# Optimization experiments

Measured on AMD Instinct MI355X. Metric: run time of the kernel, lower is better.

Reference implementation:

```python
import jax, jax.numpy as jnp
import numpy as np

T, N, E = 8, 5000, 160000
IN_DIM, HID, H = 64, 128, 8
D = HID // H  # head dim = 16
NC = 2
EPS = 1e-5


def layer_norm(x, g, b):
    mu = jnp.mean(x, axis=-1, keepdims=True)
    var = jnp.mean((x - mu) ** 2, axis=-1, keepdims=True)
    return (x - mu) / jnp.sqrt(var + EPS) * g + b


def setup_inputs() -> dict:
    key = jax.random.key(0)
    ks = jax.random.split(key, 24)
    p = {}
    p["x"] = jax.random.normal(ks[0], (T, N, IN_DIM), dtype=jnp.float32)
    p["edge_index"] = jax.random.randint(ks[1], (T, 2, E), 0, N, dtype=jnp.int32)
    p["noise"] = jax.random.normal(ks[2], (N, HID), dtype=jnp.float32)
    def w(k, shape, fan_in):
        return jax.random.normal(k, shape, dtype=jnp.float32) * (1.0 / np.sqrt(fan_in))
    p["W_proj"] = w(ks[3], (IN_DIM, HID), IN_DIM)
    p["b_proj"] = jnp.zeros((HID,), jnp.float32)
    p["W_gat"] = w(ks[4], (HID, HID), HID)
    p["a_src"] = w(ks[5], (H, D), D)
    p["a_dst"] = w(ks[6], (H, D), D)
    p["b_gat"] = jnp.zeros((HID,), jnp.float32)
    p["g1"] = jnp.ones((HID,), jnp.float32)
    p["be1"] = jnp.zeros((HID,), jnp.float32)
    p["W_qkv"] = w(ks[7], (3 * HID, HID), HID)
    p["b_qkv"] = jnp.zeros((3 * HID,), jnp.float32)
    p["W_o"] = w(ks[8], (HID, HID), HID)
    p["b_o"] = jnp.zeros((HID,), jnp.float32)
    p["g2"] = jnp.ones((HID,), jnp.float32)
    p["be2"] = jnp.zeros((HID,), jnp.float32)
    p["Wc1"] = w(ks[9], (HID, HID), HID)
    p["bc1"] = jnp.zeros((HID,), jnp.float32)
    p["gc"] = jnp.ones((HID,), jnp.float32)
    p["bec"] = jnp.zeros((HID,), jnp.float32)
    p["Wc2"] = w(ks[10], (HID, NC), HID)
    p["bc2"] = jnp.array([0.0, 0.1], jnp.float32)
    return p


def reference(x, edge_index, noise, W_proj, b_proj, W_gat, a_src, a_dst, b_gat,
              g1, be1, W_qkv, b_qkv, W_o, b_o, g2, be2,
              Wc1, bc1, gc, bec, Wc2, bc2):
    # per-timestep projection + ReLU: [T, N, HID]
    h = jax.nn.relu(x @ W_proj + b_proj)

    loop = jnp.arange(N, dtype=edge_index.dtype)

    def gat(h_t, ei):  # h_t: [N, HID], ei: [2, E]
        src = jnp.concatenate([ei[0], loop])  # add self loops
        dst = jnp.concatenate([ei[1], loop])
        xh = (h_t @ W_gat).reshape(N, H, D)          # [N, H, D]
        a_s = jnp.sum(xh * a_src, axis=-1)           # [N, H]
        a_d = jnp.sum(xh * a_dst, axis=-1)           # [N, H]
        e = jax.nn.leaky_relu(a_s[src] + a_d[dst], 0.2)  # [E', H]
        m = jax.ops.segment_max(e, dst, num_segments=N)
        ex = jnp.exp(e - m[dst])
        s = jax.ops.segment_sum(ex, dst, num_segments=N)
        alpha = ex / (s[dst] + 1e-16)                # segment softmax per dst/head
        out = jax.ops.segment_sum(xh[src] * alpha[..., None], dst, num_segments=N)
        return out.reshape(N, HID) + b_gat

    feats = jax.vmap(gat)(h, edge_index)             # [T, N, HID]
    nf = jnp.transpose(feats, (1, 0, 2))             # [N, T, HID] (node = batch)

    nrm = layer_norm(nf, g1, be1)
    qkv = nrm @ W_qkv.T + b_qkv                      # [N, T, 3*HID]
    q, k, v = jnp.split(qkv, 3, axis=-1)
    def heads(t):
        return t.reshape(N, T, H, D).transpose(0, 2, 1, 3)  # [N, H, T, D]
    q, k, v = heads(q), heads(k), heads(v)
    scores = jnp.einsum('nhqd,nhkd->nhqk', q, k) / jnp.sqrt(jnp.float32(D))
    attn = jax.nn.softmax(scores, axis=-1)
    ta = jnp.einsum('nhqk,nhkd->nhqd', attn, v)
    ta = ta.transpose(0, 2, 1, 3).reshape(N, T, HID) @ W_o.T + b_o

    fused = layer_norm(nf + ta, g2, be2)
    emb = fused[:, -1, :]                            # [N, HID]

    node_ids = jnp.arange(N, dtype=jnp.float32) / N
    div = jnp.sin(node_ids * 6.28) * 0.1             # [N]
    emb = emb + div[:, None] + noise * 0.05          # eval noise scale

    h1 = emb @ Wc1 + bc1
    h1 = jax.nn.gelu(layer_norm(h1, gc, bec), approximate=False)
    logits = h1 @ Wc2 + bc2                          # [N, 2]
    sinu = jnp.sin(jnp.arange(N, dtype=jnp.float32) * 0.5) * 0.2
    logits = logits.at[:, 1].add(sinu)
    return emb, logits
```

## Files before the change

kernel.cpp:

```cpp
#include <hip/hip_runtime.h>
#include <math.h>

#define T 8
#define N 5000
#define E 160000
#define EN (E + N)
#define IN_DIM 64
#define HID 128
#define H 8
#define D 16
#define NC 2
#define MT 32
#define NB 4
#define NRR 8
#define NCHK 32
#define RSZ ((N + NRR - 1) / NRR)
#define CSZ ((EN + NCHK - 1) / NCHK)

__device__ __forceinline__ float leaky(float e) { return (e >= 0.0f) ? e : 0.2f * e; }

__global__ __launch_bounds__(256) void k_pg(const float* __restrict__ x,
                                            const float* __restrict__ Wp,
                                            const float* __restrict__ bp,
                                            const float* __restrict__ Wg,
                                            const float* __restrict__ asrc,
                                            const float* __restrict__ adst,
                                            float* __restrict__ xh,
                                            float* __restrict__ a_s,
                                            float* __restrict__ a_d,
                                            int* __restrict__ cursor) {
    __shared__ float xt[MT][IN_DIM];
    __shared__ float ht[MT][HID + 1];
    int row0 = blockIdx.x * MT;
    int tid = threadIdx.x;

    {
        int gi = blockIdx.x * 256 + tid;
        if (gi < T * N) cursor[gi] = 0;
    }

    for (int idx = tid; idx < MT * IN_DIM; idx += 256) {
        int r = idx >> 6, k = idx & 63;
        xt[r][k] = x[(size_t)(row0 + r) * IN_DIM + k];
    }
    __syncthreads();

    int cg = tid & 31;
    int rg = tid >> 5;
    int c0 = cg * 4, r0 = rg * 4;

    {
        float4 b4 = *(const float4*)(bp + c0);
        float a00=b4.x,a01=b4.y,a02=b4.z,a03=b4.w;
        float a10=b4.x,a11=b4.y,a12=b4.z,a13=b4.w;
        float a20=b4.x,a21=b4.y,a22=b4.z,a23=b4.w;
        float a30=b4.x,a31=b4.y,a32=b4.z,a33=b4.w;
        for (int k = 0; k < IN_DIM; ++k) {
            float4 w = *(const float4*)(Wp + (size_t)k * HID + c0);
            float x0 = xt[r0 + 0][k], x1 = xt[r0 + 1][k];
            float x2 = xt[r0 + 2][k], x3 = xt[r0 + 3][k];
            a00 += x0*w.x; a01 += x0*w.y; a02 += x0*w.z; a03 += x0*w.w;
            a10 += x1*w.x; a11 += x1*w.y; a12 += x1*w.z; a13 += x1*w.w;
            a20 += x2*w.x; a21 += x2*w.y; a22 += x2*w.z; a23 += x2*w.w;
            a30 += x3*w.x; a31 += x3*w.y; a32 += x3*w.z; a33 += x3*w.w;
        }
        ht[r0+0][c0+0]=fmaxf(a00,0.f); ht[r0+0][c0+1]=fmaxf(a01,0.f);
        ht[r0+0][c0+2]=fmaxf(a02,0.f); ht[r0+0][c0+3]=fmaxf(a03,0.f);
        ht[r0+1][c0+0]=fmaxf(a10,0.f); ht[r0+1][c0+1]=fmaxf(a11,0.f);
        ht[r0+1][c0+2]=fmaxf(a12,0.f); ht[r0+1][c0+3]=fmaxf(a13,0.f);
        ht[r0+2][c0+0]=fmaxf(a20,0.f); ht[r0+2][c0+1]=fmaxf(a21,0.f);
        ht[r0+2][c0+2]=fmaxf(a22,0.f); ht[r0+2][c0+3]=fmaxf(a23,0.f);
        ht[r0+3][c0+0]=fmaxf(a30,0.f); ht[r0+3][c0+1]=fmaxf(a31,0.f);
        ht[r0+3][c0+2]=fmaxf(a32,0.f); ht[r0+3][c0+3]=fmaxf(a33,0.f);
    }
    __syncthreads();

    float a00=0,a01=0,a02=0,a03=0, a10=0,a11=0,a12=0,a13=0;
    float a20=0,a21=0,a22=0,a23=0, a30=0,a31=0,a32=0,a33=0;
    for (int k = 0; k < HID; ++k) {
        float4 w = *(const float4*)(Wg + (size_t)k * HID + c0);
        float h0 = ht[r0 + 0][k], h1 = ht[r0 + 1][k];
        float h2 = ht[r0 + 2][k], h3 = ht[r0 + 3][k];
        a00 += h0*w.x; a01 += h0*w.y; a02 += h0*w.z; a03 += h0*w.w;
        a10 += h1*w.x; a11 += h1*w.y; a12 += h1*w.z; a13 += h1*w.w;
        a20 += h2*w.x; a21 += h2*w.y; a22 += h2*w.z; a23 += h2*w.w;
        a30 += h3*w.x; a31 += h3*w.y; a32 += h3*w.z; a33 += h3*w.w;
    }
    {
        float4 v;
        v.x=a00; v.y=a01; v.z=a02; v.w=a03;
        *(float4*)(xh + (size_t)(row0 + r0 + 0) * HID + c0) = v;
        v.x=a10; v.y=a11; v.z=a12; v.w=a13;
        *(float4*)(xh + (size_t)(row0 + r0 + 1) * HID + c0) = v;
        v.x=a20; v.y=a21; v.z=a22; v.w=a23;
        *(float4*)(xh + (size_t)(row0 + r0 + 2) * HID + c0) = v;
        v.x=a30; v.y=a31; v.z=a32; v.w=a33;
        *(float4*)(xh + (size_t)(row0 + r0 + 3) * HID + c0) = v;
    }
    __syncthreads();
    ht[r0+0][c0+0]=a00; ht[r0+0][c0+1]=a01; ht[r0+0][c0+2]=a02; ht[r0+0][c0+3]=a03;
    ht[r0+1][c0+0]=a10; ht[r0+1][c0+1]=a11; ht[r0+1][c0+2]=a12; ht[r0+1][c0+3]=a13;
    ht[r0+2][c0+0]=a20; ht[r0+2][c0+1]=a21; ht[r0+2][c0+2]=a22; ht[r0+2][c0+3]=a23;
    ht[r0+3][c0+0]=a30; ht[r0+3][c0+1]=a31; ht[r0+3][c0+2]=a32; ht[r0+3][c0+3]=a33;
    __syncthreads();

    {
        int r = tid >> 3, hh = tid & 7;
        float s1 = 0.0f, s2 = 0.0f;
        #pragma unroll
        for (int d = 0; d < D; ++d) {
            float v = ht[r][hh * D + d];
            s1 += v * asrc[hh * D + d];
            s2 += v * adst[hh * D + d];
        }
        a_s[(size_t)(row0 + r) * H + hh] = s1;
        a_d[(size_t)(row0 + r) * H + hh] = s2;
    }
}

__global__ void k_tr(const float* __restrict__ W_qkv, const float* __restrict__ W_o,
                     float* __restrict__ WTq, float* __restrict__ WoT) {
    int idx = blockIdx.x * 256 + threadIdx.x;
    if (idx < 384 * 128) {
        int j = idx >> 7, c = idx & 127;
        WTq[c * 384 + j] = W_qkv[idx];
    } else if (idx < 384 * 128 + 128 * 128) {
        int r = idx - 384 * 128;
        int j = r >> 7, k = r & 127;
        WoT[k * 128 + j] = W_o[r];
    }
}

__global__ __launch_bounds__(256) void k_hist(const int* __restrict__ ei,
                                              int* __restrict__ cursor) {
    __shared__ int hist[N];
    int t = blockIdx.x >> 3;
    int chunk = blockIdx.x & 7;
    int tid = threadIdx.x;

    for (int i = tid; i < N; i += 256) hist[i] = 0;
    __syncthreads();

    const int CS = (EN + 7) / 8;
    int i0 = chunk * CS;
    int i1 = (i0 + CS < EN) ? i0 + CS : EN;
    const int* drow = ei + (size_t)(2 * t + 1) * E;
    for (int i = i0 + tid; i < i1; i += 256) {
        int d = (i < E) ? drow[i] : (i - E);
        atomicAdd(&hist[d], 1);
    }
    __syncthreads();

    int* cur = cursor + t * N;
    for (int i = tid; i < N; i += 256) {
        int c = hist[i];
        if (c) atomicAdd(&cur[i], c);
    }
}

__global__ void k_scan(int* __restrict__ cursor, int* __restrict__ offs) {
    __shared__ int part[256];
    int t = blockIdx.x;
    int tid = threadIdx.x;
    const int CH = 20;
    int begin = tid * CH;
    int sum = 0;
    for (int k = 0; k < CH; ++k) {
        int i = begin + k;
        if (i < N) sum += cursor[t * N + i];
    }
    part[tid] = sum;
    __syncthreads();
    if (tid == 0) {
        int run = 0;
        for (int i = 0; i < 256; ++i) { int v = part[i]; part[i] = run; run += v; }
        offs[t * (N + 1) + N] = run;
    }
    __syncthreads();
    int run = part[tid];
    for (int k = 0; k < CH; ++k) {
        int i = begin + k;
        if (i < N) {
            int cnt = cursor[t * N + i];
            offs[t * (N + 1) + i] = run;
            cursor[t * N + i] = run;
            run += cnt;
        }
    }
}

__global__ __launch_bounds__(256) void k_scatter(const int* __restrict__ ei,
                                                 int* __restrict__ cursor,
                                                 int* __restrict__ csr_src) {
    int idx = blockIdx.x;
    int g = idx & 63;
    int c = idx >> 6;
    int t = g >> 3;
    int r = g & 7;
    int lo = r * RSZ;
    int hi = (lo + RSZ < N) ? lo + RSZ : N;
    int i0 = c * CSZ;
    int i1 = (i0 + CSZ < EN) ? i0 + CSZ : EN;

    const int* srow = ei + (size_t)(2 * t) * E;
    const int* drow = srow + E;
    int* cur = cursor + t * N;
    int* csb = csr_src + (size_t)t * EN;

    for (int i = i0 + threadIdx.x; i < i1; i += 256) {
        int s, d;
        if (i < E) { d = drow[i]; s = srow[i]; }
        else       { s = d = i - E; }
        if (d >= lo && d < hi) {
            int pos = atomicAdd(&cur[d], 1);
            csb[pos] = s;
        }
    }
}

__global__ __launch_bounds__(128) void k_aggc(
        const int* __restrict__ offs, const int* __restrict__ csr_src,
        const float* __restrict__ a_s, const float* __restrict__ a_d,
        const float* __restrict__ xh, const float* __restrict__ b_gat,
        const float* __restrict__ g1, const float* __restrict__ be1,
        float* __restrict__ nrm, float* __restrict__ xlast_g) {
    int b = blockIdx.x;
    int t = b & 7;
    int dst = b >> 3;
    int tid = threadIdx.x;

    int o0 = offs[t * (N + 1) + dst];
    int o1 = offs[t * (N + 1) + dst + 1];
    int deg = o1 - o0;
    const int* esrc = csr_src + (size_t)t * EN + o0;
    const float* as_b = a_s + (size_t)t * N * H;
    const float* ad_b = a_d + (size_t)t * N * H;
    const float* xh_b = xh + (size_t)t * N * HID;

    __shared__ float lal[16][H];
    __shared__ int   lsrc[16];
    __shared__ float ws_s[2][H];
    __shared__ float pacc[2][HID];
    __shared__ float red[128];

    int eh_e = tid >> 3, eh_h = tid & 7;
    int el = tid >> 5, cg = tid & 31;
    int hg = cg >> 2;
    float adh_e = ad_b[dst * H + eh_h];

    float4 acc = {0.0f, 0.0f, 0.0f, 0.0f};
    float wpart = 0.0f;

    int ntile = (deg + 15) >> 4;
    for (int tt = 0; tt < ntile; ++tt) {
        int ej = (tt << 4) + eh_e;
        float w = 0.0f;
        int src = 0;
        if (ej < deg) {
            src = esrc[ej];
            w = expf(leaky(as_b[src * H + eh_h] + adh_e));
        }
        if (eh_h == 0) lsrc[eh_e] = src;
        lal[eh_e][eh_h] = w;
        wpart += w;
        __syncthreads();
        #pragma unroll
        for (int jj = 0; jj < 4; ++jj) {
            int j = (jj << 2) + el;
            int s = lsrc[j];
            float l = lal[j][hg];
            float4 v = *(const float4*)(xh_b + (size_t)s * HID + (cg << 2));
            acc.x += l * v.x; acc.y += l * v.y;
            acc.z += l * v.z; acc.w += l * v.w;
        }
        __syncthreads();
    }

    {
        float w = wpart;
        w += __shfl_xor(w, 8);
        w += __shfl_xor(w, 16);
        w += __shfl_xor(w, 32);
        if ((tid & 63) < 8) ws_s[tid >> 6][eh_h] = w;
    }
    acc.x += __shfl_xor(acc.x, 32);
    acc.y += __shfl_xor(acc.y, 32);
    acc.z += __shfl_xor(acc.z, 32);
    acc.w += __shfl_xor(acc.w, 32);
    if (!(tid & 32)) *(float4*)&pacc[tid >> 6][(tid & 31) << 2] = acc;
    __syncthreads();

    int hh = tid >> 4;
    float wsum = ws_s[0][hh] + ws_s[1][hh];
    float val = (pacc[0][tid] + pacc[1][tid]) / (wsum + 1e-16f);

    float v = val + b_gat[tid];
    red[tid] = v;
    __syncthreads();
    if (tid < 64) {
        float s = red[tid] + red[tid + 64];
        #pragma unroll
        for (int m = 1; m < 64; m <<= 1) s += __shfl_xor(s, m);
        if (tid == 0) red[0] = s;
    }
    __syncthreads();
    float mu = red[0] * (1.0f / HID);
    __syncthreads();
    float dv = v - mu;
    red[tid] = dv * dv;
    __syncthreads();
    if (tid < 64) {
        float s = red[tid] + red[tid + 64];
        #pragma unroll
        for (int m = 1; m < 64; m <<= 1) s += __shfl_xor(s, m);
        if (tid == 0) red[0] = s;
    }
    __syncthreads();
    float rstd = rsqrtf(red[0] * (1.0f / HID) + 1e-5f);

    nrm[(size_t)(dst * T + t) * HID + tid] = dv * rstd * g1[tid] + be1[tid];
    if (t == T - 1) xlast_g[(size_t)dst * HID + tid] = v;
}

__global__ __launch_bounds__(256) void k_fuse(
        const float* __restrict__ nrm,
        const float* __restrict__ WTq,
        const float* __restrict__ b_qkv,
        const float* __restrict__ xlast_g,
        const float* __restrict__ WoT,
        const float* __restrict__ b_o,
        const float* __restrict__ g2, const float* __restrict__ be2,
        const float* __restrict__ noise, float* __restrict__ out) {
    __shared__ float at[NB * T][HID];
    __shared__ float ql[NB][HID];
    __shared__ float ws[8][384];
    float* ta_s = &at[0][0];

    int n0 = blockIdx.x * NB;
    int tid = threadIdx.x;
    int cg = tid & 31, rg = tid >> 5;
    int c0 = cg * 4, r0 = rg * 4;
    int u = rg >> 1;

    {
        const float* srcp = nrm + (size_t)n0 * T * HID;
        for (int idx = tid; idx < NB * T * 32; idx += 256) {
            int r = idx >> 5, c4 = (idx & 31) << 2;
            *(float4*)&at[r][c4] = *(const float4*)(srcp + (size_t)r * HID + c4);
        }
    }

    float ka[4][4], va[4][4], qa[4];
    {
        float4 bk = *(const float4*)(b_qkv + 128 + c0);
        float4 bv = *(const float4*)(b_qkv + 256 + c0);
        #pragma unroll
        for (int i = 0; i < 4; ++i) {
            ka[i][0] = bk.x; ka[i][1] = bk.y; ka[i][2] = bk.z; ka[i][3] = bk.w;
            va[i][0] = bv.x; va[i][1] = bv.y; va[i][2] = bv.z; va[i][3] = bv.w;
        }
        if (rg < 4) {
            float4 bq = *(const float4*)(b_qkv + c0);
            qa[0] = bq.x; qa[1] = bq.y; qa[2] = bq.z; qa[3] = bq.w;
        } else {
            qa[0] = qa[1] = qa[2] = qa[3] = 0.0f;
        }
    }

    int f1 = 256 + tid, f2 = 512 + tid;
    int sr0 = tid / 96,  sc0 = (tid - sr0 * 96) << 2;
    int sr1 = f1 / 96,   sc1 = (f1 - sr1 * 96) << 2;
    int sr2 = f2 / 96,   sc2 = (f2 - sr2 * 96) << 2;
    const float* wp0 = WTq + (size_t)sr0 * 384 + sc0;
    const float* wp1 = WTq + (size_t)sr1 * 384 + sc1;
    const float* wp2 = WTq + (size_t)sr2 * 384 + sc2;
    float4 wr0 = *(const float4*)wp0;
    float4 wr1 = *(const float4*)wp1;
    float4 wr2 = *(const float4*)wp2;
    __syncthreads();

    const float* atq = at[(rg & 3) * T + (T - 1)];

    for (int kc = 0; kc < 16; ++kc) {
        if (kc) __syncthreads();
        *(float4*)&ws[sr0][sc0] = wr0;
        *(float4*)&ws[sr1][sc1] = wr1;
        *(float4*)&ws[sr2][sc2] = wr2;
        if (kc < 15) {
            int off = (kc + 1) * 8 * 384;
            wr0 = *(const float4*)(wp0 + off);
            wr1 = *(const float4*)(wp1 + off);
            wr2 = *(const float4*)(wp2 + off);
        }
        __syncthreads();

        #pragma unroll
        for (int kk = 0; kk < 8; kk += 4) {
            int k = kc * 8 + kk;
            float4 e0 = *(const float4*)&at[r0 + 0][k];
            float4 e1 = *(const float4*)&at[r0 + 1][k];
            float4 e2 = *(const float4*)&at[r0 + 2][k];
            float4 e3 = *(const float4*)&at[r0 + 3][k];
            float e0a[4] = {e0.x, e0.y, e0.z, e0.w};
            float e1a[4] = {e1.x, e1.y, e1.z, e1.w};
            float e2a[4] = {e2.x, e2.y, e2.z, e2.w};
            float e3a[4] = {e3.x, e3.y, e3.z, e3.w};
            float eqa[4] = {0.f, 0.f, 0.f, 0.f};
            if (rg < 4) {
                float4 eq = *(const float4*)&atq[k];
                eqa[0] = eq.x; eqa[1] = eq.y; eqa[2] = eq.z; eqa[3] = eq.w;
            }
            #pragma unroll
            for (int j = 0; j < 4; ++j) {
                float4 wk = *(const float4*)&ws[kk + j][128 + c0];
                float4 wv = *(const float4*)&ws[kk + j][256 + c0];
                float x0 = e0a[j], x1 = e1a[j], x2 = e2a[j], x3 = e3a[j];
                ka[0][0] += x0*wk.x; ka[0][1] += x0*wk.y; ka[0][2] += x0*wk.z; ka[0][3] += x0*wk.w;
                ka[1][0] += x1*wk.x; ka[1][1] += x1*wk.y; ka[1][2] += x1*wk.z; ka[1][3] += x1*wk.w;
                ka[2][0] += x2*wk.x; ka[2][1] += x2*wk.y; ka[2][2] += x2*wk.z; ka[2][3] += x2*wk.w;
                ka[3][0] += x3*wk.x; ka[3][1] += x3*wk.y; ka[3][2] += x3*wk.z; ka[3][3] += x3*wk.w;
                va[0][0] += x0*wv.x; va[0][1] += x0*wv.y; va[0][2] += x0*wv.z; va[0][3] += x0*wv.w;
                va[1][0] += x1*wv.x; va[1][1] += x1*wv.y; va[1][2] += x1*wv.z; va[1][3] += x1*wv.w;
                va[2][0] += x2*wv.x; va[2][1] += x2*wv.y; va[2][2] += x2*wv.z; va[2][3] += x2*wv.w;
                va[3][0] += x3*wv.x; va[3][1] += x3*wv.y; va[3][2] += x3*wv.z; va[3][3] += x3*wv.w;
                if (rg < 4) {
                    float4 wq = *(const float4*)&ws[kk + j][c0];
                    float xq = eqa[j];
                    qa[0] += xq*wq.x; qa[1] += xq*wq.y; qa[2] += xq*wq.z; qa[3] += xq*wq.w;
                }
            }
        }
    }
    __syncthreads();

    if (rg < 4) {
        float4 q4; q4.x = qa[0]; q4.y = qa[1]; q4.z = qa[2]; q4.w = qa[3];
        *(float4*)&ql[rg][c0] = q4;
    }
    __syncthreads();

    float p0, p1, p2, p3;
    {
        float4 q4 = *(const float4*)&ql[u][c0];
        float ps[4];
        #pragma unroll
        for (int i = 0; i < 4; ++i) {
            float s = q4.x * ka[i][0] + q4.y * ka[i][1]
                    + q4.z * ka[i][2] + q4.w * ka[i][3];
            s += __shfl_xor(s, 1);
            s += __shfl_xor(s, 2);
            ps[i] = s * 0.25f;
        }
        float mx = fmaxf(fmaxf(ps[0], ps[1]), fmaxf(ps[2], ps[3]));
        mx = fmaxf(mx, __shfl_xor(mx, 32));
        float e0 = expf(ps[0] - mx), e1 = expf(ps[1] - mx);
        float e2 = expf(ps[2] - mx), e3 = expf(ps[3] - mx);
        float ssum = e0 + e1 + e2 + e3;
        ssum += __shfl_xor(ssum, 32);
        float inv = 1.0f / ssum;
        p0 = (e0 * va[0][0] + e1 * va[1][0] + e2 * va[2][0] + e3 * va[3][0]) * inv;
        p1 = (e0 * va[0][1] + e1 * va[1][1] + e2 * va[2][1] + e3 * va[3][1]) * inv;
        p2 = (e0 * va[0][2] + e1 * va[1][2] + e2 * va[2][2] + e3 * va[3][2]) * inv;
        p3 = (e0 * va[0][3] + e1 * va[1][3] + e2 * va[2][3] + e3 * va[3][3]) * inv;
        p0 += __shfl_xor(p0, 32);
        p1 += __shfl_xor(p1, 32);
        p2 += __shfl_xor(p2, 32);
        p3 += __shfl_xor(p3, 32);
    }
    if (!(tid & 32)) {
        float4 t4; t4.x = p0; t4.y = p1; t4.z = p2; t4.w = p3;
        *(float4*)&ta_s[u * 128 + c0] = t4;
    }
    __syncthreads();

    {
        int uu = tid >> 6, c = tid & 63;
        int n = n0 + uu;
        float o0 = b_o[c], o1 = b_o[c + 64];
        const float* tar = ta_s + uu * 128;
        #pragma unroll 8
        for (int k = 0; k < HID; k += 4) {
            float t0 = tar[k], t1 = tar[k+1], t2 = tar[k+2], t3 = tar[k+3];
            o0 += t0 * WoT[(size_t)(k+0)*128 + c]  + t1 * WoT[(size_t)(k+1)*128 + c]
                + t2 * WoT[(size_t)(k+2)*128 + c]  + t3 * WoT[(size_t)(k+3)*128 + c];
            o1 += t0 * WoT[(size_t)(k+0)*128 + c+64] + t1 * WoT[(size_t)(k+1)*128 + c+64]
                + t2 * WoT[(size_t)(k+2)*128 + c+64] + t3 * WoT[(size_t)(k+3)*128 + c+64];
        }
        float xa = xlast_g[(size_t)n * HID + c];
        float xb = xlast_g[(size_t)n * HID + c + 64];
        float x2a = xa + o0, x2b = xb + o1;
        float s = x2a + x2b, qs = x2a * x2a + x2b * x2b;
        #pragma unroll
        for (int m = 1; m < 64; m <<= 1) {
            s  += __shfl_xor(s, m);
            qs += __shfl_xor(qs, m);
        }
        float mu = s * (1.0f / HID);
        float var = qs * (1.0f / HID) - mu * mu;
        float rstd = rsqrtf(var + 1e-5f);
        float dv = sinf(((float)n / (float)N) * 6.28f) * 0.1f;
        out[(size_t)n * HID + c] =
            (x2a - mu) * rstd * g2[c] + be2[c] + dv
            + noise[(size_t)n * HID + c] * 0.05f;
        out[(size_t)n * HID + c + 64] =
            (x2b - mu) * rstd * g2[c + 64] + be2[c + 64] + dv
            + noise[(size_t)n * HID + c + 64] * 0.05f;
    }
}

__global__ __launch_bounds__(256) void k_cls(const float* __restrict__ emb,
                                             const float* __restrict__ Wc1,
                                             const float* __restrict__ bc1,
                                             const float* __restrict__ gc,
                                             const float* __restrict__ bec,
                                             const float* __restrict__ Wc2,
                                             const float* __restrict__ bc2,
                                             float* __restrict__ out) {
    __shared__ float et[MT][HID];
    __shared__ float h1t[MT][HID + 1];
    int row0 = blockIdx.x * MT;
    int tid = threadIdx.x;

    for (int idx = tid; idx < MT * HID; idx += 256) {
        int r = idx >> 7, c = idx & 127;
        int row = row0 + r;
        et[r][c] = (row < N) ? emb[(size_t)row * HID + c] : 0.0f;
    }
    __syncthreads();

    {
        int cg = tid & 31, rg = tid >> 5;
        int c0 = cg * 4, r0 = rg * 4;
        float4 b4 = *(const float4*)(bc1 + c0);
        float a00=b4.x,a01=b4.y,a02=b4.z,a03=b4.w;
        float a10=b4.x,a11=b4.y,a12=b4.z,a13=b4.w;
        float a20=b4.x,a21=b4.y,a22=b4.z,a23=b4.w;
        float a30=b4.x,a31=b4.y,a32=b4.z,a33=b4.w;
        for (int k = 0; k < HID; ++k) {
            float4 w = *(const float4*)(Wc1 + (size_t)k * HID + c0);
            float e0 = et[r0 + 0][k], e1 = et[r0 + 1][k];
            float e2 = et[r0 + 2][k], e3 = et[r0 + 3][k];
            a00 += e0*w.x; a01 += e0*w.y; a02 += e0*w.z; a03 += e0*w.w;
            a10 += e1*w.x; a11 += e1*w.y; a12 += e1*w.z; a13 += e1*w.w;
            a20 += e2*w.x; a21 += e2*w.y; a22 += e2*w.z; a23 += e2*w.w;
            a30 += e3*w.x; a31 += e3*w.y; a32 += e3*w.z; a33 += e3*w.w;
        }
        h1t[r0+0][c0+0]=a00; h1t[r0+0][c0+1]=a01; h1t[r0+0][c0+2]=a02; h1t[r0+0][c0+3]=a03;
        h1t[r0+1][c0+0]=a10; h1t[r0+1][c0+1]=a11; h1t[r0+1][c0+2]=a12; h1t[r0+1][c0+3]=a13;
        h1t[r0+2][c0+0]=a20; h1t[r0+2][c0+1]=a21; h1t[r0+2][c0+2]=a22; h1t[r0+2][c0+3]=a23;
        h1t[r0+3][c0+0]=a30; h1t[r0+3][c0+1]=a31; h1t[r0+3][c0+2]=a32; h1t[r0+3][c0+3]=a33;
    }
    __syncthreads();

    {
        int r = tid >> 3, l = tid & 7;
        float p = 0.0f;
        #pragma unroll
        for (int k = 0; k < 16; ++k) p += h1t[r][l + 8 * k];
        #pragma unroll
        for (int m = 1; m < 8; m <<= 1) p += __shfl_xor(p, m);
        float mu = p * (1.0f / HID);
        float v = 0.0f;
        #pragma unroll
        for (int k = 0; k < 16; ++k) { float d = h1t[r][l + 8 * k] - mu; v += d * d; }
        #pragma unroll
        for (int m = 1; m < 8; m <<= 1) v += __shfl_xor(v, m);
        float rstd = rsqrtf(v * (1.0f / HID) + 1e-5f);
        #pragma unroll
        for (int k = 0; k < 16; ++k) {
            int c = l + 8 * k;
            float lnv = (h1t[r][c] - mu) * rstd * gc[c] + bec[c];
            h1t[r][c] = 0.5f * lnv * (1.0f + erff(lnv * 0.70710678118f));
        }
    }
    __syncthreads();

    if (tid < MT * NC) {
        int r = tid >> 1, j = tid & 1;
        int row = row0 + r;
        if (row < N) {
            float acc = bc2[j];
            #pragma unroll 8
            for (int c = 0; c < HID; ++c) acc += h1t[r][c] * Wc2[c * NC + j];
            if (j == 1) acc += sinf((float)row * 0.5f) * 0.2f;
            out[(size_t)N * HID + (size_t)row * NC + j] = acc;
        }
    }
}

extern "C" void kernel_launch(void* const* d_in, const int* in_sizes, int n_in,
                              void* d_out, int out_size, void* d_ws, size_t ws_size,
                              hipStream_t stream) {
    const float* x      = (const float*)d_in[0];
    const int*   ei     = (const int*)d_in[1];
    const float* noise  = (const float*)d_in[2];
    const float* W_proj = (const float*)d_in[3];
    const float* b_proj = (const float*)d_in[4];
    const float* W_gat  = (const float*)d_in[5];
    const float* a_src  = (const float*)d_in[6];
    const float* a_dst  = (const float*)d_in[7];
    const float* b_gat  = (const float*)d_in[8];
    const float* g1     = (const float*)d_in[9];
    const float* be1    = (const float*)d_in[10];
    const float* W_qkv  = (const float*)d_in[11];
    const float* b_qkv  = (const float*)d_in[12];
    const float* W_o    = (const float*)d_in[13];
    const float* b_o    = (const float*)d_in[14];
    const float* g2     = (const float*)d_in[15];
    const float* be2    = (const float*)d_in[16];
    const float* Wc1    = (const float*)d_in[17];
    const float* bc1    = (const float*)d_in[18];
    const float* gc     = (const float*)d_in[19];
    const float* bec    = (const float*)d_in[20];
    const float* Wc2    = (const float*)d_in[21];
    const float* bc2    = (const float*)d_in[22];
    float* out = (float*)d_out;

    float* xh     = (float*)d_ws;
    float* nrm    = xh + 5120000;
    float* a_s    = nrm + 5120000;
    float* a_d    = a_s + 320000;
    int*   offs    = (int*)(a_d + 320000);
    int*   cursor  = offs + 40008;
    int*   csr_src = cursor + 40000;
    float* WTq    = (float*)(csr_src + 1320000);
    float* WoT    = WTq + 49152;
    float* xlastg = WoT + 16384;

    k_tr<<<(384 * 128 + 128 * 128 + 255) / 256, 256, 0, stream>>>(W_qkv, W_o, WTq, WoT);

    k_pg<<<T * N / MT, 256, 0, stream>>>(x, W_proj, b_proj, W_gat, a_src, a_dst,
                                         xh, a_s, a_d, cursor);

    k_hist<<<T * 8, 256, 0, stream>>>(ei, cursor);
    k_scan<<<T, 256, 0, stream>>>(cursor, offs);
    k_scatter<<<64 * NCHK, 256, 0, stream>>>(ei, cursor, csr_src);

    k_aggc<<<T * N, 128, 0, stream>>>(offs, csr_src, a_s, a_d, xh,
                                      b_gat, g1, be1, nrm, xlastg);

    k_fuse<<<N / NB, 256, 0, stream>>>(nrm, WTq, b_qkv, xlastg, WoT, b_o,
                                       g2, be2, noise, out);

    k_cls<<<(N + MT - 1) / MT, 256, 0, stream>>>(out, Wc1, bc1, gc, bec, Wc2, bc2, out);
}
```

Before: 372.9 us.

## Process eight nodes per block in fused attention with one warp per node

The fused temporal-attention kernel now handles 8 nodes per block, with each 32-lane warp owning one node and all T timesteps. Each thread keeps K/V accumulators for all 8 timesteps plus Q for the last one, so the q staging buffer, its extra syncs and the cross-half-wave shuffles go away. The output projection and layernorm now use float4 loads and stores, one warp per node. The register-prefetched weight staging is dropped in favour of direct loads followed by a sync, which may expose global latency and raise register pressure (about 68 accumulators per thread). It also halves the grid size.

```diff
diff --git a/kernel.cpp b/kernel.cpp
--- a/kernel.cpp
+++ b/kernel.cpp
@@ -11,7 +11,7 @@
 #define D 16
 #define NC 2
 #define MT 32
-#define NB 4
+#define NB 8
 #define NRR 8
 #define NCHK 32
 #define RSZ ((N + NRR - 1) / NRR)
@@ -332,15 +332,14 @@
         const float* __restrict__ g2, const float* __restrict__ be2,
         const float* __restrict__ noise, float* __restrict__ out) {
     __shared__ float at[NB * T][HID];
-    __shared__ float ql[NB][HID];
     __shared__ float ws[8][384];
     float* ta_s = &at[0][0];
 
     int n0 = blockIdx.x * NB;
     int tid = threadIdx.x;
     int cg = tid & 31, rg = tid >> 5;
-    int c0 = cg * 4, r0 = rg * 4;
-    int u = rg >> 1;
+    int c0 = cg * 4;
+    int r0 = rg * T;
 
     {
         const float* srcp = nrm + (size_t)n0 * T * HID;
@@ -350,161 +349,115 @@
         }
     }
 
-    float ka[4][4], va[4][4], qa[4];
+    float ka[T][4], va[T][4], qa[4];
     {
         float4 bk = *(const float4*)(b_qkv + 128 + c0);
         float4 bv = *(const float4*)(b_qkv + 256 + c0);
-        #pragma unroll
-        for (int i = 0; i < 4; ++i) {
+        float4 bq = *(const float4*)(b_qkv + c0);
+        #pragma unroll
+        for (int i = 0; i < T; ++i) {
             ka[i][0] = bk.x; ka[i][1] = bk.y; ka[i][2] = bk.z; ka[i][3] = bk.w;
             va[i][0] = bv.x; va[i][1] = bv.y; va[i][2] = bv.z; va[i][3] = bv.w;
         }
-        if (rg < 4) {
-            float4 bq = *(const float4*)(b_qkv + c0);
-            qa[0] = bq.x; qa[1] = bq.y; qa[2] = bq.z; qa[3] = bq.w;
-        } else {
-            qa[0] = qa[1] = qa[2] = qa[3] = 0.0f;
-        }
-    }
-
-    int f1 = 256 + tid, f2 = 512 + tid;
-    int sr0 = tid / 96,  sc0 = (tid - sr0 * 96) << 2;
-    int sr1 = f1 / 96,   sc1 = (f1 - sr1 * 96) << 2;
-    int sr2 = f2 / 96,   sc2 = (f2 - sr2 * 96) << 2;
-    const float* wp0 = WTq + (size_t)sr0 * 384 + sc0;
-    const float* wp1 = WTq + (size_t)sr1 * 384 + sc1;
-    const float* wp2 = WTq + (size_t)sr2 * 384 + sc2;
-    float4 wr0 = *(const float4*)wp0;
-    float4 wr1 = *(const float4*)wp1;
-    float4 wr2 = *(const float4*)wp2;
-    __syncthreads();
-
-    const float* atq = at[(rg & 3) * T + (T - 1)];
+        qa[0] = bq.x; qa[1] = bq.y; qa[2] = bq.z; qa[3] = bq.w;
+    }
 
     for (int kc = 0; kc < 16; ++kc) {
-        if (kc) __syncthreads();
-        *(float4*)&ws[sr0][sc0] = wr0;
-        *(float4*)&ws[sr1][sc1] = wr1;
-        *(float4*)&ws[sr2][sc2] = wr2;
-        if (kc < 15) {
-            int off = (kc + 1) * 8 * 384;
-            wr0 = *(const float4*)(wp0 + off);
-            wr1 = *(const float4*)(wp1 + off);
-            wr2 = *(const float4*)(wp2 + off);
+        #pragma unroll
+        for (int j = 0; j < 3; ++j) {
+            int f = j * 256 + tid;
+            int row = f / 96;
+            int cc = (f - row * 96) << 2;
+            *(float4*)&ws[row][cc] =
+                *(const float4*)(WTq + (size_t)(kc * 8 + row) * 384 + cc);
         }
         __syncthreads();
 
         #pragma unroll
-        for (int kk = 0; kk < 8; kk += 4) {
-            int k = kc * 8 + kk;
-            float4 e0 = *(const float4*)&at[r0 + 0][k];
-            float4 e1 = *(const float4*)&at[r0 + 1][k];
-            float4 e2 = *(const float4*)&at[r0 + 2][k];
-            float4 e3 = *(const float4*)&at[r0 + 3][k];
-            float e0a[4] = {e0.x, e0.y, e0.z, e0.w};
-            float e1a[4] = {e1.x, e1.y, e1.z, e1.w};
-            float e2a[4] = {e2.x, e2.y, e2.z, e2.w};
-            float e3a[4] = {e3.x, e3.y, e3.z, e3.w};
-            float eqa[4] = {0.f, 0.f, 0.f, 0.f};
-            if (rg < 4) {
-                float4 eq = *(const float4*)&atq[k];
-                eqa[0] = eq.x; eqa[1] = eq.y; eqa[2] = eq.z; eqa[3] = eq.w;
-            }
+        for (int kk = 0; kk < 8; ++kk) {
+            float4 wk = *(const float4*)&ws[kk][128 + c0];
+            float4 wv = *(const float4*)&ws[kk][256 + c0];
+            float4 wq = *(const float4*)&ws[kk][c0];
+            const float* atc = &at[r0][0] + kc * 8 + kk;
             #pragma unroll
-            for (int j = 0; j < 4; ++j) {
-                float4 wk = *(const float4*)&ws[kk + j][128 + c0];
-                float4 wv = *(const float4*)&ws[kk + j][256 + c0];
-                float x0 = e0a[j], x1 = e1a[j], x2 = e2a[j], x3 = e3a[j];
-                ka[0][0] += x0*wk.x; ka[0][1] += x0*wk.y; ka[0][2] += x0*wk.z; ka[0][3] += x0*wk.w;
-                ka[1][0] += x1*wk.x; ka[1][1] += x1*wk.y; ka[1][2] += x1*wk.z; ka[1][3] += x1*wk.w;
-                ka[2][0] += x2*wk.x; ka[2][1] += x2*wk.y; ka[2][2] += x2*wk.z; ka[2][3] += x2*wk.w;
-                ka[3][0] += x3*wk.x; ka[3][1] += x3*wk.y; ka[3][2] += x3*wk.z; ka[3][3] += x3*wk.w;
-                va[0][0] += x0*wv.x; va[0][1] += x0*wv.y; va[0][2] += x0*wv.z; va[0][3] += x0*wv.w;
-                va[1][0] += x1*wv.x; va[1][1] += x1*wv.y; va[1][2] += x1*wv.z; va[1][3] += x1*wv.w;
-                va[2][0] += x2*wv.x; va[2][1] += x2*wv.y; va[2][2] += x2*wv.z; va[2][3] += x2*wv.w;
-                va[3][0] += x3*wv.x; va[3][1] += x3*wv.y; va[3][2] += x3*wv.z; va[3][3] += x3*wv.w;
-                if (rg < 4) {
-                    float4 wq = *(const float4*)&ws[kk + j][c0];
-                    float xq = eqa[j];
-                    qa[0] += xq*wq.x; qa[1] += xq*wq.y; qa[2] += xq*wq.z; qa[3] += xq*wq.w;
+            for (int i = 0; i < T; ++i) {
+                float x = atc[i * HID];
+                ka[i][0] += x*wk.x; ka[i][1] += x*wk.y;
+                ka[i][2] += x*wk.z; ka[i][3] += x*wk.w;
+                va[i][0] += x*wv.x; va[i][1] += x*wv.y;
+                va[i][2] += x*wv.z; va[i][3] += x*wv.w;
+                if (i == T - 1) {
+                    qa[0] += x*wq.x; qa[1] += x*wq.y;
+                    qa[2] += x*wq.z; qa[3] += x*wq.w;
                 }
             }
         }
-    }
-    __syncthreads();
-
-    if (rg < 4) {
-        float4 q4; q4.x = qa[0]; q4.y = qa[1]; q4.z = qa[2]; q4.w = qa[3];
-        *(float4*)&ql[rg][c0] = q4;
-    }
-    __syncthreads();
-
-    float p0, p1, p2, p3;
-    {
-        float4 q4 = *(const float4*)&ql[u][c0];
-        float ps[4];
-        #pragma unroll
-        for (int i = 0; i < 4; ++i) {
-            float s = q4.x * ka[i][0] + q4.y * ka[i][1]
-                    + q4.z * ka[i][2] + q4.w * ka[i][3];
+        __syncthreads();
+    }
+
+    {
+        float ps[T];
+        #pragma unroll
+        for (int t = 0; t < T; ++t) {
+            float s = qa[0]*ka[t][0] + qa[1]*ka[t][1]
+                    + qa[2]*ka[t][2] + qa[3]*ka[t][3];
             s += __shfl_xor(s, 1);
             s += __shfl_xor(s, 2);
-            ps[i] = s * 0.25f;
-        }
-        float mx = fmaxf(fmaxf(ps[0], ps[1]), fmaxf(ps[2], ps[3]));
-        mx = fmaxf(mx, __shfl_xor(mx, 32));
-        float e0 = expf(ps[0] - mx), e1 = expf(ps[1] - mx);
-        float e2 = expf(ps[2] - mx), e3 = expf(ps[3] - mx);
-        float ssum = e0 + e1 + e2 + e3;
-        ssum += __shfl_xor(ssum, 32);
+            ps[t] = s * 0.25f;
+        }
+        float mx = ps[0];
+        #pragma unroll
+        for (int t = 1; t < T; ++t) mx = fmaxf(mx, ps[t]);
+        float ssum = 0.0f;
+        float ex[T];
+        #pragma unroll
+        for (int t = 0; t < T; ++t) { ex[t] = expf(ps[t] - mx); ssum += ex[t]; }
         float inv = 1.0f / ssum;
-        p0 = (e0 * va[0][0] + e1 * va[1][0] + e2 * va[2][0] + e3 * va[3][0]) * inv;
-        p1 = (e0 * va[0][1] + e1 * va[1][1] + e2 * va[2][1] + e3 * va[3][1]) * inv;
-        p2 = (e0 * va[0][2] + e1 * va[1][2] + e2 * va[2][2] + e3 * va[3][2]) * inv;
-        p3 = (e0 * va[0][3] + e1 * va[1][3] + e2 * va[2][3] + e3 * va[3][3]) * inv;
-        p0 += __shfl_xor(p0, 32);
-        p1 += __shfl_xor(p1, 32);
-        p2 += __shfl_xor(p2, 32);
-        p3 += __shfl_xor(p3, 32);
-    }
-    if (!(tid & 32)) {
-        float4 t4; t4.x = p0; t4.y = p1; t4.z = p2; t4.w = p3;
-        *(float4*)&ta_s[u * 128 + c0] = t4;
-    }
-    __syncthreads();
-
-    {
-        int uu = tid >> 6, c = tid & 63;
-        int n = n0 + uu;
-        float o0 = b_o[c], o1 = b_o[c + 64];
-        const float* tar = ta_s + uu * 128;
-        #pragma unroll 8
-        for (int k = 0; k < HID; k += 4) {
-            float t0 = tar[k], t1 = tar[k+1], t2 = tar[k+2], t3 = tar[k+3];
-            o0 += t0 * WoT[(size_t)(k+0)*128 + c]  + t1 * WoT[(size_t)(k+1)*128 + c]
-                + t2 * WoT[(size_t)(k+2)*128 + c]  + t3 * WoT[(size_t)(k+3)*128 + c];
-            o1 += t0 * WoT[(size_t)(k+0)*128 + c+64] + t1 * WoT[(size_t)(k+1)*128 + c+64]
-                + t2 * WoT[(size_t)(k+2)*128 + c+64] + t3 * WoT[(size_t)(k+3)*128 + c+64];
-        }
-        float xa = xlast_g[(size_t)n * HID + c];
-        float xb = xlast_g[(size_t)n * HID + c + 64];
-        float x2a = xa + o0, x2b = xb + o1;
-        float s = x2a + x2b, qs = x2a * x2a + x2b * x2b;
-        #pragma unroll
-        for (int m = 1; m < 64; m <<= 1) {
+        float p0 = 0.f, p1 = 0.f, p2 = 0.f, p3 = 0.f;
+        #pragma unroll
+        for (int t = 0; t < T; ++t) {
+            float e = ex[t];
+            p0 += e * va[t][0]; p1 += e * va[t][1];
+            p2 += e * va[t][2]; p3 += e * va[t][3];
+        }
+        float4 t4; t4.x = p0 * inv; t4.y = p1 * inv; t4.z = p2 * inv; t4.w = p3 * inv;
+        *(float4*)&ta_s[rg * 128 + c0] = t4;
+    }
+    __syncthreads();
+
+    {
+        int n = n0 + rg;
+        float4 bo = *(const float4*)(b_o + c0);
+        float o0 = bo.x, o1 = bo.y, o2 = bo.z, o3 = bo.w;
+        const float* tar = ta_s + rg * 128;
+        #pragma unroll 4
+        for (int k = 0; k < HID; ++k) {
+            float tv = tar[k];
+            float4 w = *(const float4*)(WoT + (size_t)k * 128 + c0);
+            o0 += tv * w.x; o1 += tv * w.y; o2 += tv * w.z; o3 += tv * w.w;
+        }
+        float4 xl = *(const float4*)(xlast_g + (size_t)n * HID + c0);
+        float x0 = xl.x + o0, x1 = xl.y + o1, x2 = xl.z + o2, x3 = xl.w + o3;
+        float s = x0 + x1 + x2 + x3;
+        float qs = x0*x0 + x1*x1 + x2*x2 + x3*x3;
+        #pragma unroll
+        for (int m = 1; m < 32; m <<= 1) {
             s  += __shfl_xor(s, m);
             qs += __shfl_xor(qs, m);
         }
         float mu = s * (1.0f / HID);
         float var = qs * (1.0f / HID) - mu * mu;
         float rstd = rsqrtf(var + 1e-5f);
-        float dv = sinf(((float)n / (float)N) * 6.28f) * 0.1f;
-        out[(size_t)n * HID + c] =
-            (x2a - mu) * rstd * g2[c] + be2[c] + dv
-            + noise[(size_t)n * HID + c] * 0.05f;
-        out[(size_t)n * HID + c + 64] =
-            (x2b - mu) * rstd * g2[c + 64] + be2[c + 64] + dv
-            + noise[(size_t)n * HID + c + 64] * 0.05f;
+        float dvv = sinf(((float)n / (float)N) * 6.28f) * 0.1f;
+        float4 gg = *(const float4*)(g2 + c0);
+        float4 bb = *(const float4*)(be2 + c0);
+        float4 nz = *(const float4*)(noise + (size_t)n * HID + c0);
+        float4 r;
+        r.x = (x0 - mu) * rstd * gg.x + bb.x + dvv + nz.x * 0.05f;
+        r.y = (x1 - mu) * rstd * gg.y + bb.y + dvv + nz.y * 0.05f;
+        r.z = (x2 - mu) * rstd * gg.z + bb.z + dvv + nz.z * 0.05f;
+        r.w = (x3 - mu) * rstd * gg.w + bb.w + dvv + nz.w * 0.05f;
+        *(float4*)(out + (size_t)n * HID + c0) = r;
     }
 }
 
```

Result: no change. 372.5 us (-0.1%).
